# Kernel optimization log

Measured on AMD Instinct MI355X. Metric: run time of the kernel, lower is better.

## Reference

```python
import jax, jax.numpy as jnp
import numpy as np

B, T, P, D = 32, 8, 196, 768
M = 10
NUM_CLASSES = 100
NUM_IDX = 98
P_MASK = 0.5


def setup_inputs() -> dict:
    key = jax.random.key(0)
    ks = jax.random.split(key, 16)
    s = 0.02
    inp = {
        'visual': jax.random.normal(ks[0], (B, T * P, D), jnp.float32),
        'audio': jax.random.normal(ks[1], (B, D), jnp.float32),
        'causal': jax.random.normal(ks[2], (B, M, D), jnp.float32),
        'random_mask': jax.random.uniform(ks[3], (B, T, P, D)) < P_MASK,
        'Wa': jax.random.normal(ks[4], (D, D), jnp.float32) * s,
        'ba': jnp.zeros((D,), jnp.float32),
        'Wv': jax.random.normal(ks[5], (D, D), jnp.float32) * s,
        'bv': jnp.zeros((D,), jnp.float32),
        'Waa': jax.random.normal(ks[6], (D, D), jnp.float32) * s,
        'baa': jnp.zeros((D,), jnp.float32),
        'Wav': jax.random.normal(ks[7], (D, D), jnp.float32) * s,
        'bav': jnp.zeros((D,), jnp.float32),
        'Wf': jax.random.normal(ks[8], (D, D), jnp.float32) * s,
        'bf': jnp.zeros((D,), jnp.float32),
        'Wf2': jax.random.normal(ks[9], (D, 1), jnp.float32) * s,
        'bf2': jnp.zeros((1,), jnp.float32),
        'Wc': jax.random.normal(ks[10], (D, NUM_CLASSES), jnp.float32) * s,
        'bc': jnp.zeros((NUM_CLASSES,), jnp.float32),
        'causal_param': jnp.zeros((1,), jnp.float32),
    }
    return inp


def reference(visual, audio, causal, random_mask, Wa, ba, Wv, bv, Waa, baa,
              Wav, bav, Wf, bf, Wf2, bf2, Wc, bc, causal_param):
    vis = visual.reshape(visual.shape[0], T, -1, D)  # [B,8,196,768]

    # causal_intervention_mean_feature4
    cp = jax.nn.sigmoid(causal_param)                 # soft_clamp2, [1]
    feats = causal @ Wf + bf                          # [B,M,D]
    feats2 = jnp.swapaxes(causal @ Wf2 + bf2, 1, 2)   # [B,1,M]
    fw = jax.nn.softmax(jnp.tanh(feats), axis=1)      # [B,M,D]
    ci = jnp.einsum('bom,bmd->bd', feats2, fw * causal)  # bmm + squeeze
    audio2 = cp * ci + audio                          # [B,D]

    # audio_visual_attention1
    pa = jnp.tanh(audio2 @ Waa + baa)                 # [B,D]
    pv = jnp.tanh(vis @ Wav + bav)                    # [B,T,P,D]
    sscore = pv * pa[:, None, None, :]                # einsum ijkd,id->ijkd
    sattn = jax.nn.softmax(sscore, axis=2)            # softmax over patches
    patch = jnp.sum(sattn, axis=-1)                   # [B,T,P]
    thresh = jnp.sort(patch, axis=-1)[:, :, NUM_IDX]  # per (b,t) threshold
    spa_mask = patch < thresh[:, :, None]             # [B,T,P]
    final_mask = ~(spa_mask[..., None] & random_mask) # [B,T,P,D]
    sfilt = jnp.where(final_mask, sattn, 0.0)

    sav = jnp.sum(sfilt * pv, axis=2)                 # [B,T,D]
    tattn = jax.nn.softmax(sav * pa[:, None, :], axis=1)

    vp = jnp.sum(sfilt * vis, axis=2)                 # [B,T,D]
    vp = jnp.sum(tattn * vp, axis=1)                  # [B,D]

    af = jax.nn.relu(audio2 @ Wa + ba)
    vf = jax.nn.relu(vp @ Wv + bv)
    logits = (af + vf) @ Wc + bc                      # [B,num_classes]
    return logits
```

## Files before the change

### kernel.cpp

```cpp
#include <hip/hip_runtime.h>
#include <hip/hip_bf16.h>
#include <hip/hip_fp16.h>
#include <math.h>

#define BB 32
#define TT 8
#define PP 196
#define DD 768
#define MM 10
#define NCLS 100
#define NIDX 98

typedef __attribute__((ext_vector_type(8))) short short8v;
typedef __attribute__((ext_vector_type(4))) float float4v;

__device__ __forceinline__ float fast_tanh(float x) {
    float e = __expf(2.0f * x);
    return 1.0f - 2.0f / (e + 1.0f);
}
__device__ __forceinline__ unsigned short f2bf(float x) {
    __hip_bfloat16 h = __float2bfloat16(x);
    return *(unsigned short*)&h;
}
__device__ __forceinline__ float bf2f(unsigned short h) {
    return __uint_as_float(((unsigned)h) << 16);
}
__device__ __forceinline__ unsigned short f2h(float x) {
    __half h = __float2half(x);
    return *(unsigned short*)&h;
}
__device__ __forceinline__ float h2f(unsigned short u) {
    __half h = *(__half*)&u;
    return __half2float(h);
}

__global__ __launch_bounds__(768) void k_prep_all(
    const float* __restrict__ vis, unsigned short* __restrict__ visb,
    const unsigned int* __restrict__ rm, int* __restrict__ mode,
    const float* __restrict__ Wav, unsigned short* __restrict__ Wht,
    const float* __restrict__ causal, const float* __restrict__ Wf,
    const float* __restrict__ Wf2,
    float* __restrict__ pf, float* __restrict__ pf2) {
    int t = threadIdx.x;
    int bid = blockIdx.x;
    if (bid < 1024) {
        const size_t NC = (size_t)BB * TT * PP * DD / 8;
        size_t gid = (size_t)bid * 768 + t;
        for (size_t i = gid; i < NC; i += 1024 * 768) {
            const float4* s = (const float4*)(vis + i * 8);
            float4 x = s[0], y = s[1];
            __hip_bfloat162 h;
            unsigned int u0, u1, u2, u3;
            h = __float22bfloat162_rn(make_float2(x.x, x.y)); u0 = *(unsigned int*)&h;
            h = __float22bfloat162_rn(make_float2(x.z, x.w)); u1 = *(unsigned int*)&h;
            h = __float22bfloat162_rn(make_float2(y.x, y.y)); u2 = *(unsigned int*)&h;
            h = __float22bfloat162_rn(make_float2(y.z, y.w)); u3 = *(unsigned int*)&h;
            uint4 o; o.x = u0; o.y = u1; o.z = u2; o.w = u3;
            ((uint4*)visb)[i] = o;
        }
        if (bid == 0) {
            __shared__ int f_ni, f_nf;
            if (t == 0) { f_ni = 0; f_nf = 0; }
            __syncthreads();
            int ni = 0, nf = 0;
            for (int i = t; i < 16384; i += 768) {
                unsigned int v = rm[i];
                ni |= (v > 1u) ? 1 : 0;
                nf |= (v != 0u && v != 0x3F800000u) ? 1 : 0;
            }
            if (ni) atomicOr(&f_ni, 1);
            if (nf) atomicOr(&f_nf, 1);
            __syncthreads();
            if (t == 0) *mode = f_ni ? (f_nf ? 2 : 1) : 0;
        }
    } else if (bid < 1600) {
        __shared__ float tile[32][33];
        int bb = bid - 1024;
        int bn = (bb % 24) * 32;
        int bk = (bb / 24) * 32;
        if (t < 256) {
            int tx = t & 31, ty = t >> 5;
            #pragma unroll
            for (int i = 0; i < 4; ++i)
                tile[ty + i * 8][tx] = Wav[(size_t)(bk + ty + i * 8) * DD + bn + tx];
        }
        __syncthreads();
        if (t < 256) {
            int tx = t & 31, ty = t >> 5;
            #pragma unroll
            for (int i = 0; i < 4; ++i) {
                int n = bn + ty + i * 8, k = bk + tx;
                Wht[(size_t)n * DD + k] = f2bf(tile[tx][ty + i * 8]);
            }
        }
    } else {
        __shared__ float cs[MM][256];
        __shared__ float red[MM][12];
        int bb = bid - 1600;
        int b = bb % 32, kc = bb / 32;
        int k0 = kc * 256;
        for (int i = t; i < MM * 256; i += 768)
            cs[i >> 8][i & 255] = causal[((size_t)b * MM + (i >> 8)) * DD + k0 + (i & 255)];
        __syncthreads();
        int wave = t >> 6, lane = t & 63;
        float w2v = (t < 256) ? Wf2[k0 + t] : 0.f;
        #pragma unroll
        for (int m = 0; m < MM; ++m) {
            float p = (t < 256) ? cs[m][t] * w2v : 0.f;
            #pragma unroll
            for (int o = 32; o > 0; o >>= 1) p += __shfl_down(p, o);
            if (lane == 0) red[m][wave] = p;
        }
        __syncthreads();
        if (t < MM) {
            float s = 0.f;
            #pragma unroll
            for (int wv = 0; wv < 4; ++wv) s += red[t][wv];
            pf2[(b * 3 + kc) * MM + t] = s;
        }
        float acc[MM];
        #pragma unroll
        for (int m = 0; m < MM; ++m) acc[m] = 0.f;
        #pragma unroll 4
        for (int k = 0; k < 256; ++k) {
            float wv = Wf[(size_t)(k0 + k) * DD + t];
            #pragma unroll
            for (int m = 0; m < MM; ++m) acc[m] = fmaf(cs[m][k], wv, acc[m]);
        }
        #pragma unroll
        for (int m = 0; m < MM; ++m)
            pf[(((size_t)b * 3 + kc) * MM + m) * DD + t] = acc[m];
    }
}

__global__ __launch_bounds__(768) void k_audio2a(
    const float* __restrict__ causal, const float* __restrict__ audio,
    const float* __restrict__ pf, const float* __restrict__ pf2,
    const float* __restrict__ bf, const float* __restrict__ bf2,
    const float* __restrict__ cparam, float* __restrict__ a2) {
    int b = blockIdx.x;
    int t = threadIdx.x;
    float cp = 1.0f / (1.0f + __expf(-cparam[0]));
    float tf[MM], f2[MM];
    float mx = -1e30f;
    #pragma unroll
    for (int m = 0; m < MM; ++m) {
        float acc = bf[t];
        float s2 = bf2[0];
        #pragma unroll
        for (int kc = 0; kc < 3; ++kc) {
            acc += pf[(((size_t)b * 3 + kc) * MM + m) * DD + t];
            s2 += pf2[(b * 3 + kc) * MM + m];
        }
        tf[m] = fast_tanh(acc);
        f2[m] = s2;
        mx = fmaxf(mx, tf[m]);
    }
    float s = 0.f;
    #pragma unroll
    for (int m = 0; m < MM; ++m) { tf[m] = __expf(tf[m] - mx); s += tf[m]; }
    float inv = 1.0f / s;
    float ci = 0.f;
    #pragma unroll
    for (int m = 0; m < MM; ++m)
        ci += f2[m] * (tf[m] * inv) * causal[((size_t)b * MM + m) * DD + t];
    a2[(size_t)b * DD + t] = cp * ci + audio[(size_t)b * DD + t];
}

__global__ __launch_bounds__(256) void k_audio2b(
    const float* __restrict__ a2,
    const float* __restrict__ Waa, const float* __restrict__ baa,
    const float* __restrict__ Wa, const float* __restrict__ ba,
    float* __restrict__ pa, float* __restrict__ af, float* __restrict__ colsum) {
    int gid0 = (blockIdx.y * 24 + blockIdx.x) * 256 + threadIdx.x;
    for (int i = gid0; i < BB * TT * DD; i += 48 * 256) colsum[i] = 0.f;
    __shared__ float a2s[16][DD + 4];
    int sel = blockIdx.y;
    const float* W = sel ? Wa : Waa;
    int t = threadIdx.x;
    int c = blockIdx.x * 32 + (t & 31);
    int slot = t >> 5;
    float bias = sel ? ba[c] : baa[c];
    #pragma unroll
    for (int g = 0; g < 2; ++g) {
        if (g) __syncthreads();
        for (int i = t; i < 16 * DD; i += 256)
            a2s[i / DD][i % DD] = a2[(size_t)(g * 16 + i / DD) * DD + i % DD];
        __syncthreads();
        float acc0 = 0.f, acc1 = 0.f;
        #pragma unroll 8
        for (int k = 0; k < DD; ++k) {
            float wv = W[(size_t)k * DD + c];
            acc0 = fmaf(a2s[slot][k], wv, acc0);
            acc1 = fmaf(a2s[slot + 8][k], wv, acc1);
        }
        int b0 = g * 16 + slot, b1 = b0 + 8;
        if (sel == 0) {
            pa[(size_t)b0 * DD + c] = fast_tanh(acc0 + bias);
            pa[(size_t)b1 * DD + c] = fast_tanh(acc1 + bias);
        } else {
            af[(size_t)b0 * DD + c] = fmaxf(acc0 + bias, 0.f);
            af[(size_t)b1 * DD + c] = fmaxf(acc1 + bias, 0.f);
        }
    }
}

__global__ __launch_bounds__(256, 2) void k_pv_mfma(
    const unsigned short* __restrict__ visb, const unsigned short* __restrict__ Wht,
    const float* __restrict__ bav, const float* __restrict__ pa,
    unsigned short* __restrict__ pvh, float* __restrict__ colsum)
{
    __shared__ unsigned short As[2][128 * 64];
    __shared__ unsigned short Bs[2][128 * 64];
    int wg = blockIdx.x;
    int lin = (wg & 7) * 294 + (wg >> 3);
    int mt = lin / 6, nt = lin % 6;
    int i0 = mt * 128, n0 = nt * 128;
    int t = threadIdx.x, w = t >> 6, l = t & 63;
    int wm = (w >> 1) * 64, wn = (w & 1) * 64;

    float4v zero4 = {0.f, 0.f, 0.f, 0.f};
    float4v acc[4][4];
    #pragma unroll
    for (int a = 0; a < 4; ++a)
        #pragma unroll
        for (int b = 0; b < 4; ++b) acc[a][b] = zero4;

    int brow[4], bcs[4];
    #pragma unroll
    for (int j = 0; j < 4; ++j) {
        int row = (w * 4 + j) * 8 + (l >> 3);
        brow[j] = row;
        bcs[j] = (l & 7) ^ (row & 7);
    }

#define STAGE(bb, wnd_)                                                          \
    {                                                                            \
        int kw_ = (wnd_) * 64;                                                   \
        _Pragma("unroll")                                                        \
        for (int j = 0; j < 4; ++j) {                                            \
            size_t aoff_ = (size_t)(i0 + brow[j]) * DD + kw_ + bcs[j] * 8;       \
            __builtin_amdgcn_global_load_lds(                                    \
                (const __attribute__((address_space(1))) unsigned int*)(visb + aoff_), \
                (__attribute__((address_space(3))) unsigned int*)&As[bb][(w * 4 + j) * 512], \
                16, 0, 0);                                                       \
            size_t boff_ = (size_t)(n0 + brow[j]) * DD + kw_ + bcs[j] * 8;       \
            __builtin_amdgcn_global_load_lds(                                    \
                (const __attribute__((address_space(1))) unsigned int*)(Wht + boff_), \
                (__attribute__((address_space(3))) unsigned int*)&Bs[bb][(w * 4 + j) * 512], \
                16, 0, 0);                                                       \
        }                                                                        \
    }

    STAGE(0, 0);
    __syncthreads();
    for (int wnd = 0; wnd < 12; ++wnd) {
        int cur = wnd & 1;
        if (wnd < 11) STAGE(cur ^ 1, wnd + 1);
        #pragma unroll
        for (int kk = 0; kk < 2; ++kk) {
            short8v ahf[4], bhf[4];
            #pragma unroll
            for (int mr = 0; mr < 4; ++mr) {
                int row = wm + mr * 16 + (l & 15);
                int c = kk * 4 + (l >> 4);
                ahf[mr] = *(const short8v*)&As[cur][row * 64 + ((c ^ (row & 7)) * 8)];
            }
            #pragma unroll
            for (int nc = 0; nc < 4; ++nc) {
                int row = wn + nc * 16 + (l & 15);
                int c = kk * 4 + (l >> 4);
                bhf[nc] = *(const short8v*)&Bs[cur][row * 64 + ((c ^ (row & 7)) * 8)];
            }
            #pragma unroll
            for (int mr = 0; mr < 4; ++mr)
                #pragma unroll
                for (int nc = 0; nc < 4; ++nc)
                    acc[mr][nc] = __builtin_amdgcn_mfma_f32_16x16x32_bf16(
                        ahf[mr], bhf[nc], acc[mr][nc], 0, 0, 0);
        }
        __syncthreads();
    }
#undef STAGE
    unsigned short* Cl = &As[0][0];
    float* cred = (float*)&Bs[0][0];
    if (t < 256) cred[t] = 0.f;
    __syncthreads();
    int bt0 = i0 / PP;
    int btbound = (bt0 + 1) * PP;
    #pragma unroll
    for (int nc = 0; nc < 4; ++nc) {
        int cl = wn + nc * 16 + (l & 15);
        int col = n0 + cl;
        float bias = bav[col];
        #pragma unroll
        for (int mr = 0; mr < 4; ++mr) {
            int lr0 = wm + mr * 16 + ((l >> 4) << 2);
            int row0 = i0 + lr0;
            int bq = row0 / (TT * PP);
            float pav = pa[(size_t)bq * DD + col];
            float esum = 0.f;
            #pragma unroll
            for (int v = 0; v < 4; ++v) {
                unsigned short pb = f2h(fast_tanh(acc[mr][nc][v] + bias));
                int lr = lr0 + v;
                int boff = lr * 256 + ((cl * 2) ^ ((lr & 7) << 4));
                *(unsigned short*)((char*)Cl + boff) = pb;
                esum += __expf(h2f(pb) * pav);
            }
            int btg = (row0 >= btbound) ? 1 : 0;
            atomicAdd(&cred[btg * 128 + cl], esum);
        }
    }
    __syncthreads();
    #pragma unroll
    for (int rb = 0; rb < 2; ++rb) {
        int lr = (t >> 2) + rb * 64;
        size_t grow = (size_t)(i0 + lr) * DD + n0;
        #pragma unroll
        for (int q = 0; q < 4; ++q) {
            int ch = (t & 3) + q * 4;
            int boff = lr * 256 + ((ch * 16) ^ ((lr & 7) << 4));
            uint4 val = *(uint4*)((char*)Cl + boff);
            *(uint4*)(pvh + grow + ch * 8) = val;
        }
    }
    if (t < 256) {
        int btg = t >> 7, cl = t & 127;
        if (btg == 0 || btbound < i0 + 128)
            atomicAdd(&colsum[(size_t)(bt0 + btg) * DD + n0 + cl], cred[t]);
    }
}

__global__ __launch_bounds__(768) void k_patch(
    const unsigned short* __restrict__ pvh, const float* __restrict__ pa,
    const float* __restrict__ colsum, unsigned char* __restrict__ spa_g) {
    int bt = blockIdx.x;
    int b = bt >> 3;
    size_t base = (size_t)bt * PP * DD;
    __shared__ float2 pi[DD];
    __shared__ float patch[PP];
    int t = threadIdx.x;
    float pav = pa[(size_t)b * DD + t];
    float inv = 1.0f / colsum[(size_t)bt * DD + t];
    pi[t] = make_float2(pav, inv);
    __syncthreads();
    int wave = t >> 6, lane = t & 63;
    for (int p = wave; p < PP; p += 12) {
        const uint2* rv = (const uint2*)(pvh + base + (size_t)p * DD);
        float sum = 0.f;
        #pragma unroll
        for (int j = lane; j < 192; j += 64) {
            uint2 v = rv[j];
            int c = j * 4;
            float2 q0 = pi[c], q1 = pi[c + 1], q2 = pi[c + 2], q3 = pi[c + 3];
            sum += __expf(h2f((unsigned short)(v.x & 0xFFFFu)) * q0.x) * q0.y
                 + __expf(h2f((unsigned short)(v.x >> 16)) * q1.x) * q1.y
                 + __expf(h2f((unsigned short)(v.y & 0xFFFFu)) * q2.x) * q2.y
                 + __expf(h2f((unsigned short)(v.y >> 16)) * q3.x) * q3.y;
        }
        #pragma unroll
        for (int o = 32; o > 0; o >>= 1) sum += __shfl_down(sum, o);
        if (lane == 0) patch[p] = sum;
    }
    __syncthreads();
    if (t < PP) {
        float x = patch[t];
        int c = 0;
        for (int q = 0; q < PP; ++q) c += (patch[q] <= x) ? 1 : 0;
        spa_g[bt * PP + t] = (c <= NIDX) ? 1 : 0;
    }
}

__global__ __launch_bounds__(768) void k_masked(
    const unsigned short* __restrict__ pvh, const unsigned short* __restrict__ visb,
    const void* __restrict__ rmask, const int* __restrict__ mode_p,
    const float* __restrict__ pa, const float* __restrict__ colsum,
    const unsigned char* __restrict__ spa_g,
    float* __restrict__ sav, float* __restrict__ vpt) {
    int bt = blockIdx.x;
    int half = blockIdx.y;
    int b = bt >> 3;
    size_t base = (size_t)bt * PP * DD;
    __shared__ unsigned char spa[PP];
    __shared__ float red_s[2][384];
    __shared__ float red_v[2][384];
    int t = threadIdx.x;
    if (t < PP) spa[t] = spa_g[bt * PP + t];
    int pg = (t >= 384) ? 1 : 0;
    int c = t - pg * 384;
    int col = half * 384 + c;
    int p0 = pg * 98, p1 = p0 + 98;
    float pav = pa[(size_t)b * DD + col];
    float inv = 1.0f / colsum[(size_t)bt * DD + col];
    __syncthreads();
    const unsigned short* pvb = pvh + base + col;
    const unsigned short* vib = visb + base + col;
    float sava = 0.f, vpa = 0.f;
    int mode = *mode_p;
    if (mode == 0) {
        const int* mb = (const int*)rmask + base + col;
        #pragma unroll 7
        for (int p = p0; p < p1; ++p) {
            float pvv = h2f(pvb[(size_t)p * DD]);
            float sa = __expf(pvv * pav) * inv;
            bool km = !(spa[p] && (mb[(size_t)p * DD] != 0));
            if (km) { sava = fmaf(sa, pvv, sava); vpa = fmaf(sa, bf2f(vib[(size_t)p * DD]), vpa); }
        }
    } else if (mode == 1) {
        const float* mb = (const float*)rmask + base + col;
        #pragma unroll 7
        for (int p = p0; p < p1; ++p) {
            float pvv = h2f(pvb[(size_t)p * DD]);
            float sa = __expf(pvv * pav) * inv;
            bool km = !(spa[p] && (mb[(size_t)p * DD] != 0.f));
            if (km) { sava = fmaf(sa, pvv, sava); vpa = fmaf(sa, bf2f(vib[(size_t)p * DD]), vpa); }
        }
    } else {
        const unsigned char* mb = (const unsigned char*)rmask + base + col;
        #pragma unroll 7
        for (int p = p0; p < p1; ++p) {
            float pvv = h2f(pvb[(size_t)p * DD]);
            float sa = __expf(pvv * pav) * inv;
            bool km = !(spa[p] && (mb[(size_t)p * DD] != 0));
            if (km) { sava = fmaf(sa, pvv, sava); vpa = fmaf(sa, bf2f(vib[(size_t)p * DD]), vpa); }
        }
    }
    red_s[pg][c] = sava;
    red_v[pg][c] = vpa;
    __syncthreads();
    if (t < 384) {
        int col2 = half * 384 + t;
        sav[(size_t)bt * DD + col2] = red_s[0][t] + red_s[1][t];
        vpt[(size_t)bt * DD + col2] = red_v[0][t] + red_v[1][t];
    }
}

__global__ __launch_bounds__(768) void k_tail_a(
    const float* __restrict__ sav, const float* __restrict__ vpt,
    const float* __restrict__ pa, float* __restrict__ vp) {
    int b = blockIdx.x;
    int t = threadIdx.x;
    float pav = pa[(size_t)b * DD + t];
    float x[TT];
    float mx = -1e30f;
    #pragma unroll
    for (int k = 0; k < TT; ++k) {
        x[k] = sav[((size_t)b * TT + k) * DD + t] * pav;
        mx = fmaxf(mx, x[k]);
    }
    float s = 0.f;
    #pragma unroll
    for (int k = 0; k < TT; ++k) { x[k] = __expf(x[k] - mx); s += x[k]; }
    float inv = 1.0f / s;
    float acc = 0.f;
    #pragma unroll
    for (int k = 0; k < TT; ++k)
        acc += x[k] * inv * vpt[((size_t)b * TT + k) * DD + t];
    vp[(size_t)b * DD + t] = acc;
}

__global__ __launch_bounds__(256) void k_tail_b(
    const float* __restrict__ vp, const float* __restrict__ af,
    const float* __restrict__ Wv, const float* __restrict__ bv,
    float* __restrict__ h) {
    __shared__ float vs[16][DD + 4];
    int t = threadIdx.x;
    int c = blockIdx.x * 32 + (t & 31);
    int slot = t >> 5;
    float bias = bv[c];
    #pragma unroll
    for (int g = 0; g < 2; ++g) {
        if (g) __syncthreads();
        for (int i = t; i < 16 * DD; i += 256)
            vs[i / DD][i % DD] = vp[(size_t)(g * 16 + i / DD) * DD + i % DD];
        __syncthreads();
        float acc0 = 0.f, acc1 = 0.f;
        #pragma unroll 8
        for (int k = 0; k < DD; ++k) {
            float wv = Wv[(size_t)k * DD + c];
            acc0 = fmaf(vs[slot][k], wv, acc0);
            acc1 = fmaf(vs[slot + 8][k], wv, acc1);
        }
        int b0 = g * 16 + slot, b1 = b0 + 8;
        h[(size_t)b0 * DD + c] = fmaxf(acc0 + bias, 0.f) + af[(size_t)b0 * DD + c];
        h[(size_t)b1 * DD + c] = fmaxf(acc1 + bias, 0.f) + af[(size_t)b1 * DD + c];
    }
}

__global__ __launch_bounds__(256) void k_tail_c(
    const float* __restrict__ h, const float* __restrict__ Wc,
    const float* __restrict__ bc, float* __restrict__ out) {
    int t = threadIdx.x;
    int c = blockIdx.x * 8 + (t & 7);
    int b = t >> 3;
    if (c >= NCLS) return;
    float acc = bc[c];
    #pragma unroll 8
    for (int k = 0; k < DD; ++k)
        acc = fmaf(h[(size_t)b * DD + k], Wc[(size_t)k * NCLS + c], acc);
    out[(size_t)b * NCLS + c] = acc;
}

extern "C" void kernel_launch(void* const* d_in, const int* in_sizes, int n_in,
                              void* d_out, int out_size, void* d_ws, size_t ws_size,
                              hipStream_t stream) {
    const float* visual = (const float*)d_in[0];
    const float* audio  = (const float*)d_in[1];
    const float* causal = (const float*)d_in[2];
    const void*  rmask  = d_in[3];
    const float* Wa   = (const float*)d_in[4];
    const float* ba   = (const float*)d_in[5];
    const float* Wv   = (const float*)d_in[6];
    const float* bv   = (const float*)d_in[7];
    const float* Waa  = (const float*)d_in[8];
    const float* baa  = (const float*)d_in[9];
    const float* Wav  = (const float*)d_in[10];
    const float* bav  = (const float*)d_in[11];
    const float* Wf   = (const float*)d_in[12];
    const float* bf   = (const float*)d_in[13];
    const float* Wf2  = (const float*)d_in[14];
    const float* bf2  = (const float*)d_in[15];
    const float* Wc   = (const float*)d_in[16];
    const float* bc   = (const float*)d_in[17];
    const float* cpar = (const float*)d_in[18];
    float* out = (float*)d_out;

    const size_t NE = (size_t)BB * TT * PP * DD;
    unsigned short* Wht = (unsigned short*)d_ws;
    float* pfreg = (float*)(Wht + (size_t)DD * DD);
    float* colsum = pfreg;
    float* savw  = colsum + (size_t)BB * TT * DD;
    float* vptw  = savw + (size_t)BB * TT * DD;
    float* vpw   = vptw + (size_t)BB * TT * DD;
    float* hw    = vpw + (size_t)BB * DD;
    unsigned char* spa_g = (unsigned char*)(hw + (size_t)BB * DD);
    float* pf    = pfreg;
    float* pf2   = pfreg + (size_t)BB * 3 * MM * DD;
    float* a2w   = pf2 + 1024;
    float* paw   = a2w + (size_t)BB * DD;
    float* afw   = paw + (size_t)BB * DD;
    int*   modew = (int*)(afw + (size_t)BB * DD);
    unsigned short* visb = (unsigned short*)(modew + 16);
    unsigned short* pvh  = visb + NE;

    k_prep_all<<<1696, 768, 0, stream>>>(visual, visb, (const unsigned int*)rmask,
                                         modew, Wav, Wht, causal, Wf, Wf2, pf, pf2);
    k_audio2a<<<BB, 768, 0, stream>>>(causal, audio, pf, pf2, bf, bf2, cpar, a2w);
    k_audio2b<<<dim3(24, 2), 256, 0, stream>>>(a2w, Waa, baa, Wa, ba, paw, afw, colsum);
    k_pv_mfma<<<2352, 256, 0, stream>>>(visb, Wht, bav, paw, pvh, colsum);
    k_patch<<<BB * TT, 768, 0, stream>>>(pvh, paw, colsum, spa_g);
    k_masked<<<dim3(BB * TT, 2), 768, 0, stream>>>(pvh, visb, rmask, modew, paw,
                                                   colsum, spa_g, savw, vptw);
    k_tail_a<<<BB, 768, 0, stream>>>(savw, vptw, paw, vpw);
    k_tail_b<<<24, 256, 0, stream>>>(vpw, afw, Wv, bv, hw);
    k_tail_c<<<13, 256, 0, stream>>>(hw, Wc, bc, out);
}
```

Baseline: 505.6 us.

## Overlap GEMM loads with partial waitcnt and fuse patch/masked kernels

The MFMA GEMM loop now issues the next stage's global-to-LDS loads, waits with a partial vmcnt, raises wave priority during the MFMA block and replaces __syncthreads with explicit waitcnt plus s_barrier. This lets loads overlap compute instead of draining them fully each iteration. Separately, k_patch and k_masked are merged into one k_spatial kernel that keeps the spatial mask in shared memory, which removes a launch and the spa_g round trip. In exchange, the masked reduction runs with 256 blocks of one column per thread over all 196 patches, which is less parallel than the previous 512-block split with two patch halves.

```diff
diff --git a/kernel.cpp b/kernel.cpp
--- a/kernel.cpp
+++ b/kernel.cpp
@@ -253,10 +253,16 @@
     }
 
     STAGE(0, 0);
-    __syncthreads();
     for (int wnd = 0; wnd < 12; ++wnd) {
         int cur = wnd & 1;
-        if (wnd < 11) STAGE(cur ^ 1, wnd + 1);
+        if (wnd < 11) {
+            STAGE(cur ^ 1, wnd + 1);
+            asm volatile("s_waitcnt vmcnt(8)" ::: "memory");
+        } else {
+            asm volatile("s_waitcnt vmcnt(0)" ::: "memory");
+        }
+        __builtin_amdgcn_s_barrier();
+        __builtin_amdgcn_s_setprio(1);
         #pragma unroll
         for (int kk = 0; kk < 2; ++kk) {
             short8v ahf[4], bhf[4];
@@ -279,7 +285,10 @@
                     acc[mr][nc] = __builtin_amdgcn_mfma_f32_16x16x32_bf16(
                         ahf[mr], bhf[nc], acc[mr][nc], 0, 0, 0);
         }
-        __syncthreads();
+        __builtin_amdgcn_s_setprio(0);
+        asm volatile("s_waitcnt lgkmcnt(0)" ::: "memory");
+        __builtin_amdgcn_sched_barrier(0);
+        __builtin_amdgcn_s_barrier();
     }
 #undef STAGE
     unsigned short* Cl = &As[0][0];
@@ -332,14 +341,17 @@
     }
 }
 
-__global__ __launch_bounds__(768) void k_patch(
-    const unsigned short* __restrict__ pvh, const float* __restrict__ pa,
-    const float* __restrict__ colsum, unsigned char* __restrict__ spa_g) {
+__global__ __launch_bounds__(768) void k_spatial(
+    const unsigned short* __restrict__ pvh, const unsigned short* __restrict__ visb,
+    const void* __restrict__ rmask, const int* __restrict__ mode_p,
+    const float* __restrict__ pa, const float* __restrict__ colsum,
+    float* __restrict__ sav, float* __restrict__ vpt) {
     int bt = blockIdx.x;
     int b = bt >> 3;
     size_t base = (size_t)bt * PP * DD;
     __shared__ float2 pi[DD];
     __shared__ float patch[PP];
+    __shared__ unsigned char spa[PP];
     int t = threadIdx.x;
     float pav = pa[(size_t)b * DD + t];
     float inv = 1.0f / colsum[(size_t)bt * DD + t];
@@ -368,72 +380,43 @@
         float x = patch[t];
         int c = 0;
         for (int q = 0; q < PP; ++q) c += (patch[q] <= x) ? 1 : 0;
-        spa_g[bt * PP + t] = (c <= NIDX) ? 1 : 0;
-    }
-}
-
-__global__ __launch_bounds__(768) void k_masked(
-    const unsigned short* __restrict__ pvh, const unsigned short* __restrict__ visb,
-    const void* __restrict__ rmask, const int* __restrict__ mode_p,
-    const float* __restrict__ pa, const float* __restrict__ colsum,
-    const unsigned char* __restrict__ spa_g,
-    float* __restrict__ sav, float* __restrict__ vpt) {
-    int bt = blockIdx.x;
-    int half = blockIdx.y;
-    int b = bt >> 3;
-    size_t base = (size_t)bt * PP * DD;
-    __shared__ unsigned char spa[PP];
-    __shared__ float red_s[2][384];
-    __shared__ float red_v[2][384];
-    int t = threadIdx.x;
-    if (t < PP) spa[t] = spa_g[bt * PP + t];
-    int pg = (t >= 384) ? 1 : 0;
-    int c = t - pg * 384;
-    int col = half * 384 + c;
-    int p0 = pg * 98, p1 = p0 + 98;
-    float pav = pa[(size_t)b * DD + col];
-    float inv = 1.0f / colsum[(size_t)bt * DD + col];
+        spa[t] = (c <= NIDX) ? 1 : 0;
+    }
     __syncthreads();
-    const unsigned short* pvb = pvh + base + col;
-    const unsigned short* vib = visb + base + col;
+    int mode = *mode_p;
+    const unsigned short* pvb = pvh + base + t;
+    const unsigned short* vib = visb + base + t;
     float sava = 0.f, vpa = 0.f;
-    int mode = *mode_p;
     if (mode == 0) {
-        const int* mb = (const int*)rmask + base + col;
-        #pragma unroll 7
-        for (int p = p0; p < p1; ++p) {
+        const int* mb = (const int*)rmask + base + t;
+        #pragma unroll 8
+        for (int p = 0; p < PP; ++p) {
             float pvv = h2f(pvb[(size_t)p * DD]);
             float sa = __expf(pvv * pav) * inv;
             bool km = !(spa[p] && (mb[(size_t)p * DD] != 0));
             if (km) { sava = fmaf(sa, pvv, sava); vpa = fmaf(sa, bf2f(vib[(size_t)p * DD]), vpa); }
         }
     } else if (mode == 1) {
-        const float* mb = (const float*)rmask + base + col;
-        #pragma unroll 7
-        for (int p = p0; p < p1; ++p) {
+        const float* mb = (const float*)rmask + base + t;
+        #pragma unroll 8
+        for (int p = 0; p < PP; ++p) {
             float pvv = h2f(pvb[(size_t)p * DD]);
             float sa = __expf(pvv * pav) * inv;
             bool km = !(spa[p] && (mb[(size_t)p * DD] != 0.f));
             if (km) { sava = fmaf(sa, pvv, sava); vpa = fmaf(sa, bf2f(vib[(size_t)p * DD]), vpa); }
         }
     } else {
-        const unsigned char* mb = (const unsigned char*)rmask + base + col;
-        #pragma unroll 7
-        for (int p = p0; p < p1; ++p) {
+        const unsigned char* mb = (const unsigned char*)rmask + base + t;
+        #pragma unroll 8
+        for (int p = 0; p < PP; ++p) {
             float pvv = h2f(pvb[(size_t)p * DD]);
             float sa = __expf(pvv * pav) * inv;
             bool km = !(spa[p] && (mb[(size_t)p * DD] != 0));
             if (km) { sava = fmaf(sa, pvv, sava); vpa = fmaf(sa, bf2f(vib[(size_t)p * DD]), vpa); }
         }
     }
-    red_s[pg][c] = sava;
-    red_v[pg][c] = vpa;
-    __syncthreads();
-    if (t < 384) {
-        int col2 = half * 384 + t;
-        sav[(size_t)bt * DD + col2] = red_s[0][t] + red_s[1][t];
-        vpt[(size_t)bt * DD + col2] = red_v[0][t] + red_v[1][t];
-    }
+    sav[(size_t)bt * DD + t] = sava;
+    vpt[(size_t)bt * DD + t] = vpa;
 }
 
 __global__ __launch_bounds__(768) void k_tail_a(
@@ -534,7 +517,6 @@
     float* vptw  = savw + (size_t)BB * TT * DD;
     float* vpw   = vptw + (size_t)BB * TT * DD;
     float* hw    = vpw + (size_t)BB * DD;
-    unsigned char* spa_g = (unsigned char*)(hw + (size_t)BB * DD);
     float* pf    = pfreg;
     float* pf2   = pfreg + (size_t)BB * 3 * MM * DD;
     float* a2w   = pf2 + 1024;
@@ -549,9 +531,8 @@
     k_audio2a<<<BB, 768, 0, stream>>>(causal, audio, pf, pf2, bf, bf2, cpar, a2w);
     k_audio2b<<<dim3(24, 2), 256, 0, stream>>>(a2w, Waa, baa, Wa, ba, paw, afw, colsum);
     k_pv_mfma<<<2352, 256, 0, stream>>>(visb, Wht, bav, paw, pvh, colsum);
-    k_patch<<<BB * TT, 768, 0, stream>>>(pvh, paw, colsum, spa_g);
-    k_masked<<<dim3(BB * TT, 2), 768, 0, stream>>>(pvh, visb, rmask, modew, paw,
-                                                   colsum, spa_g, savw, vptw);
+    k_spatial<<<BB * TT, 768, 0, stream>>>(pvh, visb, rmask, modew, paw, colsum,
+                                           savw, vptw);
     k_tail_a<<<BB, 768, 0, stream>>>(savw, vptw, paw, vpw);
     k_tail_b<<<24, 256, 0, stream>>>(vpw, afw, Wv, bv, hw);
     k_tail_c<<<13, 256, 0, stream>>>(hw, Wc, bc, out);
```

After: 555.5 us. 1.1x slower.
